# Optimization experiments

Hardware: AMD Instinct MI355X
Metric: run time of the kernel (lower is better)

The kernel has to match this reference:

```python
import jax, jax.numpy as jnp
import numpy as np

N = 200000  # number of mesh nodes (source hardcodes n; scaled to production)

def setup_inputs() -> dict:
    key = jax.random.key(0)
    ks = jax.random.split(key, 7)
    spatial = jax.random.normal(ks[0], (N, 64), dtype=jnp.float32)
    structural = jax.random.normal(ks[1], (N, 131), dtype=jnp.float32)
    neighbour = jax.random.randint(ks[2], (N, 3), 0, N, dtype=jnp.int64)
    # Conv1d(kernel_size=1) == linear layer; weights [out_c, in_c]
    Wc = jax.random.normal(ks[3], (256, 195), dtype=jnp.float32) * (1.0 / np.sqrt(195))
    bc = jax.random.normal(ks[4], (256,), dtype=jnp.float32) * 0.01
    Wa = jax.random.normal(ks[5], (256, 131), dtype=jnp.float32) * (1.0 / np.sqrt(131))
    ba = jax.random.normal(ks[6], (256,), dtype=jnp.float32) * 0.01
    return {"spatial": spatial, "structural": structural, "neighbour": neighbour,
            "Wc": Wc, "bc": bc, "Wa": Wa, "ba": ba}

def reference(spatial, structural, neighbour, Wc, bc, Wa, ba):
    # Combination1: concat(spatial[n,64], structural[n,131]) -> 1x1 conv (linear)
    a1 = jnp.concatenate([spatial, structural], axis=1)      # [n,195]
    out1 = jnp.einsum('nc,oc->no', a1, Wc) + bc               # [n,256]
    # Aggregation1: mean of self + 3 gathered neighbor feature vectors
    nbr_feats = structural[neighbour]                          # [n,3,131] gather
    vec4 = (structural + nbr_feats.sum(axis=1)) * 0.25        # [n,131]
    out2 = jnp.einsum('nc,oc->no', vec4, Wa) + ba             # [n,256]
    return (out1, out2)
```

## Files before the change

### kernel.cpp

```cpp
#include <hip/hip_runtime.h>
#include <hip/hip_bf16.h>

#define K1 195
#define K1P 224
#define K2 131
#define K2P 160
#define OC 256
#define BM 32
#define S1 232
#define S2 168
#define THREADS 512

typedef __attribute__((ext_vector_type(4))) float f32x4;
typedef __attribute__((ext_vector_type(8))) short bf16x8;
typedef __attribute__((ext_vector_type(4))) short bf16x4;

__device__ __forceinline__ short f2b(float x) {
    __hip_bfloat16 h = __float2bfloat16(x);
    return *reinterpret_cast<short*>(&h);
}

__global__ void prep_weights_v11(const float* __restrict__ Wc, const float* __restrict__ Wa,
                                 __hip_bfloat16* __restrict__ WcP, __hip_bfloat16* __restrict__ WaP) {
    int t = blockIdx.x * blockDim.x + threadIdx.x;
    const int total1 = OC * K1P;
    const int total2 = OC * K2P;
    if (t < total1) {
        int oc = t / K1P, k = t - oc * K1P;
        float v = (k < K1) ? Wc[oc * K1 + k] : 0.0f;
        WcP[t] = __float2bfloat16(v);
    } else if (t < total1 + total2) {
        int u = t - total1;
        int oc = u / K2P, k = u - oc * K2P;
        float v = (k < K2) ? Wa[oc * K2 + k] : 0.0f;
        WaP[u] = __float2bfloat16(v);
    }
}

__global__ __launch_bounds__(THREADS) void fused_mesh_v11(
        const float* __restrict__ spatial,
        const float* __restrict__ structural,
        const int* __restrict__ neighbour,
        const __hip_bfloat16* __restrict__ WcP,
        const float* __restrict__ bc,
        const __hip_bfloat16* __restrict__ WaP,
        const float* __restrict__ ba,
        float* __restrict__ out1,
        float* __restrict__ out2,
        int n) {
    __shared__ __hip_bfloat16 A1[BM][S1];
    __shared__ __hip_bfloat16 A2[BM][S2];
    __shared__ int nidx[BM * 3];

    const int t = threadIdx.x;
    const int r0 = blockIdx.x * BM;

    if (t < BM * 3) {
        size_t gi = (size_t)r0 * 3 + t;
        nidx[t] = (gi < (size_t)n * 3) ? neighbour[gi] : 0;
    }

    for (int e = t; e < BM * (K1P - K1); e += THREADS) {
        int r = e / (K1P - K1);
        int k = K1 + (e - r * (K1P - K1));
        A1[r][k] = __float2bfloat16(0.0f);
    }
    for (int e = t; e < BM * (K2P - K2); e += THREADS) {
        int r = e / (K2P - K2);
        int k = K2 + (e - r * (K2P - K2));
        A2[r][k] = __float2bfloat16(0.0f);
    }

    {
        int r  = t >> 4;
        int c0 = (t & 15) * 4;
        int rr = min(r0 + r, n - 1);
        f32x4 v = *(const f32x4*)(spatial + (size_t)rr * 64 + c0);
        bf16x4 o;
        #pragma unroll
        for (int j = 0; j < 4; ++j) o[j] = f2b(v[j]);
        *(bf16x4*)&A1[r][c0] = o;
    }
    __syncthreads();

    for (int e = t; e < BM * K2; e += THREADS) {
        int r = e / K2;
        int k = e - r * K2;
        int rr = min(r0 + r, n - 1);
        float self = structural[(size_t)rr * K2 + k];
        int n0 = nidx[r * 3 + 0];
        int n1 = nidx[r * 3 + 1];
        int n2 = nidx[r * 3 + 2];
        float v = self + structural[(size_t)n0 * K2 + k]
                       + structural[(size_t)n1 * K2 + k]
                       + structural[(size_t)n2 * K2 + k];
        A1[r][64 + k] = __float2bfloat16(self);
        A2[r][k]      = __float2bfloat16(v * 0.25f);
    }
    __syncthreads();

    const int wid  = t >> 6;
    const int lane = t & 63;
    const int lr   = lane & 15;
    const int lkc  = lane >> 4;
    const int colBase = wid * 32;

    {
        f32x4 acc[2][2];
        #pragma unroll
        for (int i = 0; i < 2; ++i)
            #pragma unroll
            for (int j = 0; j < 2; ++j)
                acc[i][j] = (f32x4){0.f, 0.f, 0.f, 0.f};

        #pragma unroll
        for (int ks = 0; ks < K1P; ks += 32) {
            bf16x8 a[2], b[2];
            #pragma unroll
            for (int rt = 0; rt < 2; ++rt)
                a[rt] = *(const bf16x8*)&A1[rt * 16 + lr][ks + lkc * 8];
            #pragma unroll
            for (int ct = 0; ct < 2; ++ct) {
                int oc = colBase + ct * 16 + lr;
                b[ct] = *(const bf16x8*)(WcP + (size_t)oc * K1P + ks + lkc * 8);
            }
            #pragma unroll
            for (int rt = 0; rt < 2; ++rt)
                #pragma unroll
                for (int ct = 0; ct < 2; ++ct)
                    acc[ct][rt] = __builtin_amdgcn_mfma_f32_16x16x32_bf16(b[ct], a[rt], acc[ct][rt], 0, 0, 0);
        }

        #pragma unroll
        for (int ct = 0; ct < 2; ++ct) {
            int oc0 = colBase + ct * 16 + lkc * 4;
            f32x4 b4 = *(const f32x4*)(bc + oc0);
            #pragma unroll
            for (int rt = 0; rt < 2; ++rt) {
                int node = r0 + rt * 16 + lr;
                if (node < n) {
                    f32x4 v = acc[ct][rt] + b4;
                    __builtin_nontemporal_store(v, (f32x4*)(out1 + (size_t)node * OC + oc0));
                }
            }
        }
    }

    {
        f32x4 acc[2][2];
        #pragma unroll
        for (int i = 0; i < 2; ++i)
            #pragma unroll
            for (int j = 0; j < 2; ++j)
                acc[i][j] = (f32x4){0.f, 0.f, 0.f, 0.f};

        #pragma unroll
        for (int ks = 0; ks < K2P; ks += 32) {
            bf16x8 a[2], b[2];
            #pragma unroll
            for (int rt = 0; rt < 2; ++rt)
                a[rt] = *(const bf16x8*)&A2[rt * 16 + lr][ks + lkc * 8];
            #pragma unroll
            for (int ct = 0; ct < 2; ++ct) {
                int oc = colBase + ct * 16 + lr;
                b[ct] = *(const bf16x8*)(WaP + (size_t)oc * K2P + ks + lkc * 8);
            }
            #pragma unroll
            for (int rt = 0; rt < 2; ++rt)
                #pragma unroll
                for (int ct = 0; ct < 2; ++ct)
                    acc[ct][rt] = __builtin_amdgcn_mfma_f32_16x16x32_bf16(b[ct], a[rt], acc[ct][rt], 0, 0, 0);
        }

        #pragma unroll
        for (int ct = 0; ct < 2; ++ct) {
            int oc0 = colBase + ct * 16 + lkc * 4;
            f32x4 b4 = *(const f32x4*)(ba + oc0);
            #pragma unroll
            for (int rt = 0; rt < 2; ++rt) {
                int node = r0 + rt * 16 + lr;
                if (node < n) {
                    f32x4 v = acc[ct][rt] + b4;
                    __builtin_nontemporal_store(v, (f32x4*)(out2 + (size_t)node * OC + oc0));
                }
            }
        }
    }
}

extern "C" void kernel_launch(void* const* d_in, const int* in_sizes, int n_in,
                              void* d_out, int out_size, void* d_ws, size_t ws_size,
                              hipStream_t stream) {
    const float* spatial    = (const float*)d_in[0];
    const float* structural = (const float*)d_in[1];
    const int*   neighbour  = (const int*)d_in[2];
    const float* Wc = (const float*)d_in[3];
    const float* bc = (const float*)d_in[4];
    const float* Wa = (const float*)d_in[5];
    const float* ba = (const float*)d_in[6];

    const int n = in_sizes[0] / 64;

    float* out1 = (float*)d_out;
    float* out2 = out1 + (size_t)n * OC;

    __hip_bfloat16* WcP = (__hip_bfloat16*)d_ws;
    __hip_bfloat16* WaP = WcP + OC * K1P;

    {
        const int total = OC * K1P + OC * K2P;
        prep_weights_v11<<<(total + 255) / 256, 256, 0, stream>>>(Wc, Wa, WcP, WaP);
    }
    {
        const int grid = (n + BM - 1) / BM;
        fused_mesh_v11<<<grid, THREADS, 0, stream>>>(spatial, structural, neighbour,
                                                     WcP, bc, WaP, ba, out1, out2, n);
    }
}
```

Baseline: 192.1 us.

## Pre-convert structural features to padded bf16 for vectorized neighbour gathers

Adds a pre-pass that converts the structural matrix to bf16 with rows padded to 136 elements. The fused kernel then gathers self and neighbour rows as 16-byte bf16x8 vectors instead of scalar fp32 loads, which is meant to cut gather traffic and the number of load instructions. The cost is an extra full pass over structural (read fp32, write bf16) plus a kernel launch. Neighbour values are now rounded to bf16 before they are summed, which slightly changes numerics. The path only runs when the workspace is large enough.

```diff
diff --git a/kernel.cpp b/kernel.cpp
--- a/kernel.cpp
+++ b/kernel.cpp
@@ -4,6 +4,7 @@
 #define K1 195
 #define K1P 224
 #define K2 131
+#define K2B 136
 #define K2P 160
 #define OC 256
 #define BM 32
@@ -14,13 +15,17 @@
 typedef __attribute__((ext_vector_type(4))) float f32x4;
 typedef __attribute__((ext_vector_type(8))) short bf16x8;
 typedef __attribute__((ext_vector_type(4))) short bf16x4;
+typedef __attribute__((ext_vector_type(2))) short bf16x2;
 
 __device__ __forceinline__ short f2b(float x) {
     __hip_bfloat16 h = __float2bfloat16(x);
     return *reinterpret_cast<short*>(&h);
 }
-
-__global__ void prep_weights_v11(const float* __restrict__ Wc, const float* __restrict__ Wa,
+__device__ __forceinline__ float b2f(short x) {
+    return __uint_as_float(((unsigned)(unsigned short)x) << 16);
+}
+
+__global__ void prep_weights_v13(const float* __restrict__ Wc, const float* __restrict__ Wa,
                                  __hip_bfloat16* __restrict__ WcP, __hip_bfloat16* __restrict__ WaP) {
     int t = blockIdx.x * blockDim.x + threadIdx.x;
     const int total1 = OC * K1P;
@@ -37,9 +42,26 @@
     }
 }
 
-__global__ __launch_bounds__(THREADS) void fused_mesh_v11(
+__global__ void prep_structB_v13(const float* __restrict__ structural,
+                                 __hip_bfloat16* __restrict__ structB, int n) {
+    int idx = blockIdx.x * blockDim.x + threadIdx.x;
+    const int ppr = K2B / 2;
+    if (idx >= n * ppr) return;
+    int r = idx / ppr;
+    int c = (idx - r * ppr) * 2;
+    float v0 = (c     < K2) ? structural[(size_t)r * K2 + c]     : 0.0f;
+    float v1 = (c + 1 < K2) ? structural[(size_t)r * K2 + c + 1] : 0.0f;
+    bf16x2 o;
+    o[0] = f2b(v0);
+    o[1] = f2b(v1);
+    *(bf16x2*)((short*)structB + (size_t)r * K2B + c) = o;
+}
+
+template<bool USE_SB>
+__global__ __launch_bounds__(THREADS) void fused_mesh_v13(
         const float* __restrict__ spatial,
         const float* __restrict__ structural,
+        const __hip_bfloat16* __restrict__ structB,
         const int* __restrict__ neighbour,
         const __hip_bfloat16* __restrict__ WcP,
         const float* __restrict__ bc,
@@ -83,19 +105,41 @@
     }
     __syncthreads();
 
-    for (int e = t; e < BM * K2; e += THREADS) {
-        int r = e / K2;
-        int k = e - r * K2;
-        int rr = min(r0 + r, n - 1);
-        float self = structural[(size_t)rr * K2 + k];
-        int n0 = nidx[r * 3 + 0];
-        int n1 = nidx[r * 3 + 1];
-        int n2 = nidx[r * 3 + 2];
-        float v = self + structural[(size_t)n0 * K2 + k]
-                       + structural[(size_t)n1 * K2 + k]
-                       + structural[(size_t)n2 * K2 + k];
-        A1[r][64 + k] = __float2bfloat16(self);
-        A2[r][k]      = __float2bfloat16(v * 0.25f);
+    if constexpr (USE_SB) {
+        for (int u = t; u < BM * 17; u += THREADS) {
+            int r = u / 17;
+            int c = (u - r * 17) * 8;
+            int rr = min(r0 + r, n - 1);
+            const short* sb = (const short*)structB;
+            bf16x8 vs = *(const bf16x8*)(sb + (size_t)rr * K2B + c);
+            *(bf16x8*)&A1[r][64 + c] = vs;
+            int n0 = nidx[r * 3 + 0];
+            int n1 = nidx[r * 3 + 1];
+            int n2 = nidx[r * 3 + 2];
+            bf16x8 v0 = *(const bf16x8*)(sb + (size_t)n0 * K2B + c);
+            bf16x8 v1 = *(const bf16x8*)(sb + (size_t)n1 * K2B + c);
+            bf16x8 v2 = *(const bf16x8*)(sb + (size_t)n2 * K2B + c);
+            bf16x8 o;
+            #pragma unroll
+            for (int j = 0; j < 8; ++j)
+                o[j] = f2b((b2f(vs[j]) + b2f(v0[j]) + b2f(v1[j]) + b2f(v2[j])) * 0.25f);
+            *(bf16x8*)&A2[r][c] = o;
+        }
+    } else {
+        for (int e = t; e < BM * K2; e += THREADS) {
+            int r = e / K2;
+            int k = e - r * K2;
+            int rr = min(r0 + r, n - 1);
+            float self = structural[(size_t)rr * K2 + k];
+            int n0 = nidx[r * 3 + 0];
+            int n1 = nidx[r * 3 + 1];
+            int n2 = nidx[r * 3 + 2];
+            float v = self + structural[(size_t)n0 * K2 + k]
+                           + structural[(size_t)n1 * K2 + k]
+                           + structural[(size_t)n2 * K2 + k];
+            A1[r][64 + k] = __float2bfloat16(self);
+            A2[r][k]      = __float2bfloat16(v * 0.25f);
+        }
     }
     __syncthreads();
 
@@ -207,13 +251,23 @@
     __hip_bfloat16* WcP = (__hip_bfloat16*)d_ws;
     __hip_bfloat16* WaP = WcP + OC * K1P;
 
+    const size_t wbytes = (size_t)(OC * K1P + OC * K2P) * sizeof(__hip_bfloat16);
+    const size_t sbytes = (size_t)n * K2B * sizeof(__hip_bfloat16);
+    const bool use_sb = (ws_size >= wbytes + sbytes);
+    __hip_bfloat16* structB = (__hip_bfloat16*)((char*)d_ws + wbytes);
+
     {
         const int total = OC * K1P + OC * K2P;
-        prep_weights_v11<<<(total + 255) / 256, 256, 0, stream>>>(Wc, Wa, WcP, WaP);
-    }
-    {
-        const int grid = (n + BM - 1) / BM;
-        fused_mesh_v11<<<grid, THREADS, 0, stream>>>(spatial, structural, neighbour,
-                                                     WcP, bc, WaP, ba, out1, out2, n);
-    }
-}
+        prep_weights_v13<<<(total + 255) / 256, 256, 0, stream>>>(Wc, Wa, WcP, WaP);
+    }
+    const int grid = (n + BM - 1) / BM;
+    if (use_sb) {
+        const int totalp = n * (K2B / 2);
+        prep_structB_v13<<<(totalp + 255) / 256, 256, 0, stream>>>(structural, structB, n);
+        fused_mesh_v13<true><<<grid, THREADS, 0, stream>>>(spatial, structural, structB, neighbour,
+                                                           WcP, bc, WaP, ba, out1, out2, n);
+    } else {
+        fused_mesh_v13<false><<<grid, THREADS, 0, stream>>>(spatial, structural, structB, neighbour,
+                                                            WcP, bc, WaP, ba, out1, out2, n);
+    }
+}
```

Result: slower. 201.9 us (+5.1%).
